# Kernel optimization log

Measured on AMD Instinct MI355X. Metric: run time of the kernel, lower is better.

Reference implementation:

```python
import jax, jax.numpy as jnp
import numpy as np

H_HT, W_HT = 26, 122      # downsampled pred grid fed to the Hough transform
NUM_ANGLE = 60            # 180 deg / 3 deg
NUM_RHO = 125             # 2*ceil(diag/2)+1, diag = sqrt(26^2+122^2)


def _make_vote_index():
    # Reproduce the structure of vote_index_26_122_3_1.mat: for each pixel
    # (h, w) and angle a, exactly one rho bin receives a vote of 1.0.
    theta = np.deg2rad(np.arange(NUM_ANGLE) * 3.0)
    ys = np.arange(H_HT) - H_HT / 2.0 + 0.5
    xs = np.arange(W_HT) - W_HT / 2.0 + 0.5
    # rho[h, w, a] = x*cos(theta_a) + y*sin(theta_a)
    rho = xs[None, :, None] * np.cos(theta)[None, None, :] \
        + ys[:, None, None] * np.sin(theta)[None, None, :]
    ri = np.clip(np.round(rho).astype(np.int64) + NUM_RHO // 2, 0, NUM_RHO - 1)
    vote = np.zeros((H_HT, W_HT, NUM_ANGLE, NUM_RHO), dtype=np.float32)
    hh, ww, aa = np.meshgrid(np.arange(H_HT), np.arange(W_HT),
                             np.arange(NUM_ANGLE), indexing='ij')
    vote[hh, ww, aa, ri] = 1.0
    return jnp.asarray(vote)


def setup_inputs() -> dict:
    key = jax.random.key(0)
    k1, k2, k3 = jax.random.split(key, 3)
    B, C = 32, 4
    ht = jax.random.uniform(k1, (B, C, NUM_ANGLE, NUM_RHO), dtype=jnp.float32)
    pred = jax.random.uniform(k2, (B, C, 288, 800), dtype=jnp.float32)
    pred_exist = jax.random.uniform(k3, (B, C), dtype=jnp.float32)
    vote_index = _make_vote_index()
    return {"ht": ht, "pred": pred, "pred_exist": pred_exist,
            "vote_index": vote_index}


def _nearest_resize(x, out_h, out_w):
    # torch F.interpolate(mode='nearest'): src = floor(dst * in/out)
    in_h, in_w = x.shape[2], x.shape[3]
    hi = jnp.floor(jnp.arange(out_h) * (in_h / out_h)).astype(jnp.int32)
    wi = jnp.floor(jnp.arange(out_w) * (in_w / out_w)).astype(jnp.int32)
    return x[:, :, hi][:, :, :, wi]


def reference(ht, pred, pred_exist, vote_index):
    B, C = ht.shape[0], ht.shape[1]
    # --- no_grad block in the original ---
    exist = (pred_exist > 0.9).astype(ht.dtype)          # [B, 4]
    exist = jnp.broadcast_to(exist[:, None, :], (B, C, 4))  # [B, C, 4]
    pred_s = _nearest_resize(pred, H_HT, W_HT)           # [B, C, 26, 122]
    # Hough-transform vote accumulation: gather pixel values into (angle, rho)
    # bins via the one-hot vote_index table.
    pred_ht = jnp.einsum('bchw,hwar->bcar', pred_s, vote_index)  # [B,C,A,R]
    idx = jnp.argmax(pred_ht.reshape(B, C, -1), axis=2)  # [B, 4]
    idx = jnp.broadcast_to(idx[:, None, :], (B, C, 4))   # [B, C, 4]
    # --- differentiable part ---
    # F.normalize(ht, dim=2, p=1): L1-normalize along the angle dim.
    l1 = jnp.sum(jnp.abs(ht), axis=2, keepdims=True)
    ht_n = ht / jnp.maximum(l1, 1e-12)
    flat = ht_n.reshape(B, C, -1)                        # [B, C, A*R]
    gathered = jnp.take_along_axis(flat, idx, axis=2)    # [B, C, 4]
    ht_max_log = -jnp.log(gathered + 1e-12)
    loss = ht_max_log * exist
    return loss.mean(axis=2).mean(axis=1)                # [B]
```

## Files before the change

kernel.cpp:

```cpp
#include <hip/hip_runtime.h>
#include <hip/hip_bf16.h>
#include <stdint.h>
#include <math.h>

#define H_HT 26
#define W_HT 122
#define NPIX (H_HT * W_HT)
#define NA 60
#define NR 125
#define NB 32
#define NC 4
#define NBC (NB * NC)
#define PH 288
#define PW 800
#define NSPLIT 16
#define PIX_PT 13

#define TR_BLKS (H_HT * 8)
#define ZERO_BLKS 4

#define WS_OFF   190336
#define WS_LIST  220608
#define WS_PREDT 601280
#define WS_PVP   2225344

__global__ __launch_bounds__(256) void setup(const float* __restrict__ pred,
                                             int* __restrict__ off,
                                             uint16_t* __restrict__ list,
                                             float* __restrict__ pred_T,
                                             unsigned long long* __restrict__ pvp) {
    const int tid = threadIdx.x;
    if (blockIdx.x < NA) {
        const int a = blockIdx.x;
        __shared__ int s_cnt[NR];
        __shared__ int sc[2][NR];
        __shared__ int s_pre[NR + 1];
        __shared__ int s_cur[NR];

        double t  = __dmul_rn((double)(a * 3), 0.017453292519943295);
        double cs = cos(t);
        double sn = sin(t);

        int rloc[PIX_PT];
#pragma unroll
        for (int k = 0; k < PIX_PT; ++k) {
            int p = tid + k * 256;
            rloc[k] = 0;
            if (p < NPIX) {
                int h = p / W_HT;
                int w = p - h * W_HT;
                double xs = (double)w - 60.5;
                double ys = (double)h - 12.5;
                double rho = __dadd_rn(__dmul_rn(xs, cs), __dmul_rn(ys, sn));
                int r = (int)rint(rho) + NR / 2;
                r = r < 0 ? 0 : (r > NR - 1 ? NR - 1 : r);
                rloc[k] = r;
            }
        }
        for (int i = tid; i < NR; i += 256) s_cnt[i] = 0;
        __syncthreads();
#pragma unroll
        for (int k = 0; k < PIX_PT; ++k) {
            int p = tid + k * 256;
            if (p < NPIX) atomicAdd(&s_cnt[rloc[k]], 1);
        }
        __syncthreads();
        if (tid < NR) sc[0][tid] = s_cnt[tid];
        __syncthreads();
        int pin = 0;
        for (int d = 1; d < NR; d <<= 1) {
            if (tid < NR) {
                int v = sc[pin][tid];
                if (tid >= d) v += sc[pin][tid - d];
                sc[pin ^ 1][tid] = v;
            }
            __syncthreads();
            pin ^= 1;
        }
        if (tid == 0) s_pre[0] = 0;
        if (tid < NR) s_pre[tid + 1] = sc[pin][tid];
        __syncthreads();
        for (int r = tid; r < NR + 1; r += 256) off[a * (NR + 1) + r] = s_pre[r];
        for (int r = tid; r < NR; r += 256) s_cur[r] = s_pre[r];
        __syncthreads();
#pragma unroll
        for (int k = 0; k < PIX_PT; ++k) {
            int p = tid + k * 256;
            if (p < NPIX) {
                int slot = atomicAdd(&s_cur[rloc[k]], 1);
                list[a * NPIX + slot] = (uint16_t)p;
            }
        }
    } else if (blockIdx.x < NA + TR_BLKS) {
        const int bidx = blockIdx.x - NA;
        const int h    = bidx >> 3;
        const int g    = bidx & 7;
        const int bc0  = g * 16;
        __shared__ float s_row[16][802];
        const float C1 = (float)(288.0 / 26.0);
        const float C2 = (float)(800.0 / 122.0);
        const int hi = (int)floorf((float)h * C1);
        for (int i = tid; i < 16 * 200; i += 256) {
            int j  = i / 200;
            int c4 = i - j * 200;
            const float4* rp = reinterpret_cast<const float4*>(
                pred + ((size_t)(bc0 + j) * PH + hi) * PW);
            float4 v = rp[c4];
            s_row[j][c4 * 4 + 0] = v.x;
            s_row[j][c4 * 4 + 1] = v.y;
            s_row[j][c4 * 4 + 2] = v.z;
            s_row[j][c4 * 4 + 3] = v.w;
        }
        __syncthreads();
        for (int idx = tid; idx < W_HT * 16; idx += 256) {
            int w = idx >> 4;
            int j = idx & 15;
            int wi = (int)floorf((float)w * C2);
            pred_T[(size_t)(h * W_HT + w) * NBC + bc0 + j] = s_row[j][wi];
        }
    } else {
        int bz = blockIdx.x - NA - TR_BLKS;
        int i0 = bz * 256 + tid;
        for (int i = i0; i < NA * NBC; i += ZERO_BLKS * 256) pvp[i] = 0ull;
    }
}

__global__ __launch_bounds__(256) void hough_T7(const float* __restrict__ pred_T,
                                                const int* __restrict__ off,
                                                const uint16_t* __restrict__ list,
                                                unsigned long long* __restrict__ pvp) {
    __shared__ uint16_t s_list[NPIX];
    __shared__ int      s_off[NR + 1];
    __shared__ float    s_v[4][32][4];
    __shared__ int      s_i[4][32][4];

    const int blk  = blockIdx.x;
    const int a    = blk / NSPLIT;
    const int q    = blk - a * NSPLIT;
    const int tid  = threadIdx.x;
    const int w    = tid >> 6;
    const int lane = tid & 63;
    const int li   = lane & 31;
    const int hw8  = (lane >> 5) * 8;

    {
        const uint32_t* src = reinterpret_cast<const uint32_t*>(list + a * NPIX);
        uint32_t* dst = reinterpret_cast<uint32_t*>(s_list);
        for (int i = tid; i < NPIX / 2; i += 256) dst[i] = src[i];
        for (int r = tid; r < NR + 1; r += 256) s_off[r] = off[a * (NR + 1) + r];
    }
    __syncthreads();

    const float4* pT4 = reinterpret_cast<const float4*>(pred_T);
    float bvx = -1.0f, bvy = -1.0f, bvz = -1.0f, bvw = -1.0f;
    int   bix = 0, biy = 0, biz = 0, biw = 0;
    for (int r = q * 4 + w; r < NR; r += 64) {
        const int o0 = s_off[r];
        const int o1 = s_off[r + 1];
        float4 c0 = {0,0,0,0}, c1 = {0,0,0,0}, c2 = {0,0,0,0}, c3 = {0,0,0,0};
        float4 c4 = {0,0,0,0}, c5 = {0,0,0,0}, c6 = {0,0,0,0}, c7 = {0,0,0,0};
        for (int j = o0; j < o1; j += 16) {
            int base = j + hw8;
            int i0 = base, i1 = base + 1, i2 = base + 2, i3 = base + 3;
            int i4 = base + 4, i5 = base + 5, i6 = base + 6, i7 = base + 7;
            float m0 = (i0 < o1) ? 1.0f : 0.0f;
            float m1 = (i1 < o1) ? 1.0f : 0.0f;
            float m2 = (i2 < o1) ? 1.0f : 0.0f;
            float m3 = (i3 < o1) ? 1.0f : 0.0f;
            float m4 = (i4 < o1) ? 1.0f : 0.0f;
            float m5 = (i5 < o1) ? 1.0f : 0.0f;
            float m6 = (i6 < o1) ? 1.0f : 0.0f;
            float m7 = (i7 < o1) ? 1.0f : 0.0f;
            int p0 = s_list[i0 < o1 ? i0 : o0];
            int p1 = s_list[i1 < o1 ? i1 : o0];
            int p2 = s_list[i2 < o1 ? i2 : o0];
            int p3 = s_list[i3 < o1 ? i3 : o0];
            int p4 = s_list[i4 < o1 ? i4 : o0];
            int p5 = s_list[i5 < o1 ? i5 : o0];
            int p6 = s_list[i6 < o1 ? i6 : o0];
            int p7 = s_list[i7 < o1 ? i7 : o0];
            float4 v0 = pT4[p0 * 32 + li];
            float4 v1 = pT4[p1 * 32 + li];
            float4 v2 = pT4[p2 * 32 + li];
            float4 v3 = pT4[p3 * 32 + li];
            float4 v4 = pT4[p4 * 32 + li];
            float4 v5 = pT4[p5 * 32 + li];
            float4 v6 = pT4[p6 * 32 + li];
            float4 v7 = pT4[p7 * 32 + li];
            c0.x = fmaf(v0.x, m0, c0.x); c0.y = fmaf(v0.y, m0, c0.y);
            c0.z = fmaf(v0.z, m0, c0.z); c0.w = fmaf(v0.w, m0, c0.w);
            c1.x = fmaf(v1.x, m1, c1.x); c1.y = fmaf(v1.y, m1, c1.y);
            c1.z = fmaf(v1.z, m1, c1.z); c1.w = fmaf(v1.w, m1, c1.w);
            c2.x = fmaf(v2.x, m2, c2.x); c2.y = fmaf(v2.y, m2, c2.y);
            c2.z = fmaf(v2.z, m2, c2.z); c2.w = fmaf(v2.w, m2, c2.w);
            c3.x = fmaf(v3.x, m3, c3.x); c3.y = fmaf(v3.y, m3, c3.y);
            c3.z = fmaf(v3.z, m3, c3.z); c3.w = fmaf(v3.w, m3, c3.w);
            c4.x = fmaf(v4.x, m4, c4.x); c4.y = fmaf(v4.y, m4, c4.y);
            c4.z = fmaf(v4.z, m4, c4.z); c4.w = fmaf(v4.w, m4, c4.w);
            c5.x = fmaf(v5.x, m5, c5.x); c5.y = fmaf(v5.y, m5, c5.y);
            c5.z = fmaf(v5.z, m5, c5.z); c5.w = fmaf(v5.w, m5, c5.w);
            c6.x = fmaf(v6.x, m6, c6.x); c6.y = fmaf(v6.y, m6, c6.y);
            c6.z = fmaf(v6.z, m6, c6.z); c6.w = fmaf(v6.w, m6, c6.w);
            c7.x = fmaf(v7.x, m7, c7.x); c7.y = fmaf(v7.y, m7, c7.y);
            c7.z = fmaf(v7.z, m7, c7.z); c7.w = fmaf(v7.w, m7, c7.w);
        }
        float sx = ((c0.x + c1.x) + (c2.x + c3.x)) + ((c4.x + c5.x) + (c6.x + c7.x));
        float sy = ((c0.y + c1.y) + (c2.y + c3.y)) + ((c4.y + c5.y) + (c6.y + c7.y));
        float sz = ((c0.z + c1.z) + (c2.z + c3.z)) + ((c4.z + c5.z) + (c6.z + c7.z));
        float sw = ((c0.w + c1.w) + (c2.w + c3.w)) + ((c4.w + c5.w) + (c6.w + c7.w));
        sx += __shfl_xor(sx, 32);
        sy += __shfl_xor(sy, 32);
        sz += __shfl_xor(sz, 32);
        sw += __shfl_xor(sw, 32);
        int gbin = a * NR + r;
        if (sx > bvx) { bvx = sx; bix = gbin; }
        if (sy > bvy) { bvy = sy; biy = gbin; }
        if (sz > bvz) { bvz = sz; biz = gbin; }
        if (sw > bvw) { bvw = sw; biw = gbin; }
    }
    if (hw8 == 0) {
        s_v[w][li][0] = bvx; s_i[w][li][0] = bix;
        s_v[w][li][1] = bvy; s_i[w][li][1] = biy;
        s_v[w][li][2] = bvz; s_i[w][li][2] = biz;
        s_v[w][li][3] = bvw; s_i[w][li][3] = biw;
    }
    __syncthreads();
    if (tid < 32) {
#pragma unroll
        for (int comp = 0; comp < 4; ++comp) {
            float m = s_v[0][tid][comp];
            int   jb = s_i[0][tid][comp];
#pragma unroll
            for (int ww = 1; ww < 4; ++ww) {
                float ov = s_v[ww][tid][comp];
                int   oi = s_i[ww][tid][comp];
                if (ov > m || (ov == m && oi < jb)) { m = ov; jb = oi; }
            }
            unsigned long long e = ((unsigned long long)__float_as_uint(m < 0.f ? 0.f : m) << 32)
                                 | (unsigned long long)(65535 - jb);
            atomicMax(&pvp[(4 * tid + comp) * NA + a], e);
        }
    }
}

__global__ __launch_bounds__(256) void loss4(const float* __restrict__ ht,
                                             const float* __restrict__ pexist,
                                             const unsigned long long* __restrict__ pvp,
                                             float* __restrict__ out) {
    __shared__ float s_sum[4];
    const int b    = blockIdx.x;
    const int tid  = threadIdx.x;
    const int k    = tid >> 6;
    const int lane = tid & 63;
    const int c    = lane >> 4;
    const int s    = lane & 15;

    unsigned long long be = 0ull;
    if (lane < NA) be = pvp[(b * 4 + k) * NA + lane];
#pragma unroll
    for (int m = 32; m > 0; m >>= 1) {
        unsigned long long oe = __shfl_xor(be, m);
        if (oe > be) be = oe;
    }
    int fidx = 65535 - (int)(be & 0xFFFFull);
    int a0 = fidx / NR;
    int r  = fidx - a0 * NR;

    const float* htc = ht + (size_t)((b * 4 + c) * NA) * NR;
    float acc = 0.0f;
#pragma unroll
    for (int t = 0; t < 4; ++t) {
        int a = s + t * 16;
        if (a < NA) acc += fabsf(htc[a * NR + r]);
    }
#pragma unroll
    for (int m = 1; m < 16; m <<= 1) acc += __shfl_xor(acc, m);

    float term = 0.0f;
    if (s == 0) {
        float l1 = fmaxf(acc, 1e-12f);
        float gg = htc[a0 * NR + r] / l1;
        float ex = (pexist[b * 4 + k] > 0.9f) ? 1.0f : 0.0f;
        term = -logf(gg + 1e-12f) * ex;
    }
#pragma unroll
    for (int m = 16; m < 64; m <<= 1) term += __shfl_xor(term, m);
    if (lane == 0) s_sum[k] = term;
    __syncthreads();
    if (tid == 0)
        out[b] = (s_sum[0] + s_sum[1] + s_sum[2] + s_sum[3]) * (1.0f / 16.0f);
}

extern "C" void kernel_launch(void* const* d_in, const int* in_sizes, int n_in,
                              void* d_out, int out_size, void* d_ws, size_t ws_size,
                              hipStream_t stream) {
    const float* ht     = (const float*)d_in[0];
    const float* pred   = (const float*)d_in[1];
    const float* pexist = (const float*)d_in[2];

    char* ws = (char*)d_ws;
    int*      off    = (int*)     (ws + WS_OFF);
    uint16_t* list   = (uint16_t*)(ws + WS_LIST);
    float*    pred_T = (float*)   (ws + WS_PREDT);
    unsigned long long* pvp = (unsigned long long*)(ws + WS_PVP);

    setup<<<NA + TR_BLKS + ZERO_BLKS, 256, 0, stream>>>(pred, off, list, pred_T, pvp);
    hough_T7<<<NA * NSPLIT, 256, 0, stream>>>(pred_T, off, list, pvp);
    loss4<<<NB, 256, 0, stream>>>(ht, pexist, pvp, (float*)d_out);
}
```

Measured before the change: 30.08 us.

## Fuse loss into Hough kernel via last-block completion counter and precompute L1

Merges the separate loss kernel into the Hough kernel. Extra blocks compute the per-(b,c,r) L1 norms of ht alongside the voting blocks, and the last block to finish, detected through an atomic counter zeroed in setup, does the argmax reduction and the final loss. This removes one kernel launch and the serial dependency of the loss kernel. In exchange it adds threadfence/atomic overhead to every block and leaves a single block doing the final serial work. It also computes L1 for all rho bins, not just the selected ones.

```diff
diff --git a/kernel.cpp b/kernel.cpp
--- a/kernel.cpp
+++ b/kernel.cpp
@@ -18,17 +18,23 @@
 
 #define TR_BLKS (H_HT * 8)
 #define ZERO_BLKS 4
-
-#define WS_OFF   190336
-#define WS_LIST  220608
-#define WS_PREDT 601280
-#define WS_PVP   2225344
+#define HB (NA * NSPLIT)
+#define L1_BLKS 120
+#define K2_BLKS (HB + L1_BLKS)
+
+#define WS_OFF   0
+#define WS_LIST  30272
+#define WS_PREDT 410944
+#define WS_PVP   2035008
+#define WS_L1    2096448
+#define WS_CNT   2352448
 
 __global__ __launch_bounds__(256) void setup(const float* __restrict__ pred,
                                              int* __restrict__ off,
                                              uint16_t* __restrict__ list,
                                              float* __restrict__ pred_T,
-                                             unsigned long long* __restrict__ pvp) {
+                                             unsigned long long* __restrict__ pvp,
+                                             unsigned int* __restrict__ cnt) {
     const int tid = threadIdx.x;
     if (blockIdx.x < NA) {
         const int a = blockIdx.x;
@@ -122,173 +128,189 @@
         int bz = blockIdx.x - NA - TR_BLKS;
         int i0 = bz * 256 + tid;
         for (int i = i0; i < NA * NBC; i += ZERO_BLKS * 256) pvp[i] = 0ull;
+        if (bz == 0 && tid == 0) *cnt = 0u;
     }
 }
 
-__global__ __launch_bounds__(256) void hough_T7(const float* __restrict__ pred_T,
-                                                const int* __restrict__ off,
-                                                const uint16_t* __restrict__ list,
-                                                unsigned long long* __restrict__ pvp) {
+__global__ __launch_bounds__(256) void hough_l1_loss(const float* __restrict__ pred_T,
+                                                     const int* __restrict__ off,
+                                                     const uint16_t* __restrict__ list,
+                                                     unsigned long long* __restrict__ pvp,
+                                                     float* __restrict__ L1t,
+                                                     unsigned int* __restrict__ cnt,
+                                                     const float* __restrict__ ht,
+                                                     const float* __restrict__ pexist,
+                                                     float* __restrict__ out) {
     __shared__ uint16_t s_list[NPIX];
     __shared__ int      s_off[NR + 1];
     __shared__ float    s_v[4][32][4];
     __shared__ int      s_i[4][32][4];
 
-    const int blk  = blockIdx.x;
-    const int a    = blk / NSPLIT;
-    const int q    = blk - a * NSPLIT;
-    const int tid  = threadIdx.x;
-    const int w    = tid >> 6;
-    const int lane = tid & 63;
-    const int li   = lane & 31;
-    const int hw8  = (lane >> 5) * 8;
-
-    {
-        const uint32_t* src = reinterpret_cast<const uint32_t*>(list + a * NPIX);
-        uint32_t* dst = reinterpret_cast<uint32_t*>(s_list);
-        for (int i = tid; i < NPIX / 2; i += 256) dst[i] = src[i];
-        for (int r = tid; r < NR + 1; r += 256) s_off[r] = off[a * (NR + 1) + r];
-    }
+    const int tid = threadIdx.x;
+
+    if (blockIdx.x < HB) {
+        const int blk  = blockIdx.x;
+        const int a    = blk / NSPLIT;
+        const int q    = blk - a * NSPLIT;
+        const int w    = tid >> 6;
+        const int lane = tid & 63;
+        const int li   = lane & 31;
+        const int hw8  = (lane >> 5) * 8;
+
+        {
+            const uint32_t* src = reinterpret_cast<const uint32_t*>(list + a * NPIX);
+            uint32_t* dst = reinterpret_cast<uint32_t*>(s_list);
+            for (int i = tid; i < NPIX / 2; i += 256) dst[i] = src[i];
+            for (int r = tid; r < NR + 1; r += 256) s_off[r] = off[a * (NR + 1) + r];
+        }
+        __syncthreads();
+
+        const float4* pT4 = reinterpret_cast<const float4*>(pred_T);
+        float bvx = -1.0f, bvy = -1.0f, bvz = -1.0f, bvw = -1.0f;
+        int   bix = 0, biy = 0, biz = 0, biw = 0;
+        for (int r = q * 4 + w; r < NR; r += 64) {
+            const int o0 = s_off[r];
+            const int o1 = s_off[r + 1];
+            float4 c0 = {0,0,0,0}, c1 = {0,0,0,0}, c2 = {0,0,0,0}, c3 = {0,0,0,0};
+            float4 c4 = {0,0,0,0}, c5 = {0,0,0,0}, c6 = {0,0,0,0}, c7 = {0,0,0,0};
+            for (int j = o0; j < o1; j += 16) {
+                int base = j + hw8;
+                int i0 = base, i1 = base + 1, i2 = base + 2, i3 = base + 3;
+                int i4 = base + 4, i5 = base + 5, i6 = base + 6, i7 = base + 7;
+                float m0 = (i0 < o1) ? 1.0f : 0.0f;
+                float m1 = (i1 < o1) ? 1.0f : 0.0f;
+                float m2 = (i2 < o1) ? 1.0f : 0.0f;
+                float m3 = (i3 < o1) ? 1.0f : 0.0f;
+                float m4 = (i4 < o1) ? 1.0f : 0.0f;
+                float m5 = (i5 < o1) ? 1.0f : 0.0f;
+                float m6 = (i6 < o1) ? 1.0f : 0.0f;
+                float m7 = (i7 < o1) ? 1.0f : 0.0f;
+                int p0 = s_list[i0 < o1 ? i0 : o0];
+                int p1 = s_list[i1 < o1 ? i1 : o0];
+                int p2 = s_list[i2 < o1 ? i2 : o0];
+                int p3 = s_list[i3 < o1 ? i3 : o0];
+                int p4 = s_list[i4 < o1 ? i4 : o0];
+                int p5 = s_list[i5 < o1 ? i5 : o0];
+                int p6 = s_list[i6 < o1 ? i6 : o0];
+                int p7 = s_list[i7 < o1 ? i7 : o0];
+                float4 v0 = pT4[p0 * 32 + li];
+                float4 v1 = pT4[p1 * 32 + li];
+                float4 v2 = pT4[p2 * 32 + li];
+                float4 v3 = pT4[p3 * 32 + li];
+                float4 v4 = pT4[p4 * 32 + li];
+                float4 v5 = pT4[p5 * 32 + li];
+                float4 v6 = pT4[p6 * 32 + li];
+                float4 v7 = pT4[p7 * 32 + li];
+                c0.x = fmaf(v0.x, m0, c0.x); c0.y = fmaf(v0.y, m0, c0.y);
+                c0.z = fmaf(v0.z, m0, c0.z); c0.w = fmaf(v0.w, m0, c0.w);
+                c1.x = fmaf(v1.x, m1, c1.x); c1.y = fmaf(v1.y, m1, c1.y);
+                c1.z = fmaf(v1.z, m1, c1.z); c1.w = fmaf(v1.w, m1, c1.w);
+                c2.x = fmaf(v2.x, m2, c2.x); c2.y = fmaf(v2.y, m2, c2.y);
+                c2.z = fmaf(v2.z, m2, c2.z); c2.w = fmaf(v2.w, m2, c2.w);
+                c3.x = fmaf(v3.x, m3, c3.x); c3.y = fmaf(v3.y, m3, c3.y);
+                c3.z = fmaf(v3.z, m3, c3.z); c3.w = fmaf(v3.w, m3, c3.w);
+                c4.x = fmaf(v4.x, m4, c4.x); c4.y = fmaf(v4.y, m4, c4.y);
+                c4.z = fmaf(v4.z, m4, c4.z); c4.w = fmaf(v4.w, m4, c4.w);
+                c5.x = fmaf(v5.x, m5, c5.x); c5.y = fmaf(v5.y, m5, c5.y);
+                c5.z = fmaf(v5.z, m5, c5.z); c5.w = fmaf(v5.w, m5, c5.w);
+                c6.x = fmaf(v6.x, m6, c6.x); c6.y = fmaf(v6.y, m6, c6.y);
+                c6.z = fmaf(v6.z, m6, c6.z); c6.w = fmaf(v6.w, m6, c6.w);
+                c7.x = fmaf(v7.x, m7, c7.x); c7.y = fmaf(v7.y, m7, c7.y);
+                c7.z = fmaf(v7.z, m7, c7.z); c7.w = fmaf(v7.w, m7, c7.w);
+            }
+            float sx = ((c0.x + c1.x) + (c2.x + c3.x)) + ((c4.x + c5.x) + (c6.x + c7.x));
+            float sy = ((c0.y + c1.y) + (c2.y + c3.y)) + ((c4.y + c5.y) + (c6.y + c7.y));
+            float sz = ((c0.z + c1.z) + (c2.z + c3.z)) + ((c4.z + c5.z) + (c6.z + c7.z));
+            float sw = ((c0.w + c1.w) + (c2.w + c3.w)) + ((c4.w + c5.w) + (c6.w + c7.w));
+            sx += __shfl_xor(sx, 32);
+            sy += __shfl_xor(sy, 32);
+            sz += __shfl_xor(sz, 32);
+            sw += __shfl_xor(sw, 32);
+            int gbin = a * NR + r;
+            if (sx > bvx) { bvx = sx; bix = gbin; }
+            if (sy > bvy) { bvy = sy; biy = gbin; }
+            if (sz > bvz) { bvz = sz; biz = gbin; }
+            if (sw > bvw) { bvw = sw; biw = gbin; }
+        }
+        if (hw8 == 0) {
+            s_v[w][li][0] = bvx; s_i[w][li][0] = bix;
+            s_v[w][li][1] = bvy; s_i[w][li][1] = biy;
+            s_v[w][li][2] = bvz; s_i[w][li][2] = biz;
+            s_v[w][li][3] = bvw; s_i[w][li][3] = biw;
+        }
+        __syncthreads();
+        if (tid < 32) {
+#pragma unroll
+            for (int comp = 0; comp < 4; ++comp) {
+                float m = s_v[0][tid][comp];
+                int   jb = s_i[0][tid][comp];
+#pragma unroll
+                for (int ww = 1; ww < 4; ++ww) {
+                    float ov = s_v[ww][tid][comp];
+                    int   oi = s_i[ww][tid][comp];
+                    if (ov > m || (ov == m && oi < jb)) { m = ov; jb = oi; }
+                }
+                unsigned long long e = ((unsigned long long)__float_as_uint(m < 0.f ? 0.f : m) << 32)
+                                     | (unsigned long long)(65535 - jb);
+                atomicMax(&pvp[(4 * tid + comp) * NA + a], e);
+            }
+        }
+    } else {
+        const int i = blockIdx.x - HB;
+        for (int e = i * 256 + tid; e < NBC * NR; e += L1_BLKS * 256) {
+            int cr = e / NR;
+            int r  = e - cr * NR;
+            const float* base = ht + (size_t)cr * NA * NR + r;
+            float s = 0.0f;
+            for (int a = 0; a < NA; ++a) s += fabsf(base[a * NR]);
+            L1t[e] = s;
+        }
+    }
+
+    __shared__ unsigned int s_last;
+    __threadfence();
     __syncthreads();
-
-    const float4* pT4 = reinterpret_cast<const float4*>(pred_T);
-    float bvx = -1.0f, bvy = -1.0f, bvz = -1.0f, bvw = -1.0f;
-    int   bix = 0, biy = 0, biz = 0, biw = 0;
-    for (int r = q * 4 + w; r < NR; r += 64) {
-        const int o0 = s_off[r];
-        const int o1 = s_off[r + 1];
-        float4 c0 = {0,0,0,0}, c1 = {0,0,0,0}, c2 = {0,0,0,0}, c3 = {0,0,0,0};
-        float4 c4 = {0,0,0,0}, c5 = {0,0,0,0}, c6 = {0,0,0,0}, c7 = {0,0,0,0};
-        for (int j = o0; j < o1; j += 16) {
-            int base = j + hw8;
-            int i0 = base, i1 = base + 1, i2 = base + 2, i3 = base + 3;
-            int i4 = base + 4, i5 = base + 5, i6 = base + 6, i7 = base + 7;
-            float m0 = (i0 < o1) ? 1.0f : 0.0f;
-            float m1 = (i1 < o1) ? 1.0f : 0.0f;
-            float m2 = (i2 < o1) ? 1.0f : 0.0f;
-            float m3 = (i3 < o1) ? 1.0f : 0.0f;
-            float m4 = (i4 < o1) ? 1.0f : 0.0f;
-            float m5 = (i5 < o1) ? 1.0f : 0.0f;
-            float m6 = (i6 < o1) ? 1.0f : 0.0f;
-            float m7 = (i7 < o1) ? 1.0f : 0.0f;
-            int p0 = s_list[i0 < o1 ? i0 : o0];
-            int p1 = s_list[i1 < o1 ? i1 : o0];
-            int p2 = s_list[i2 < o1 ? i2 : o0];
-            int p3 = s_list[i3 < o1 ? i3 : o0];
-            int p4 = s_list[i4 < o1 ? i4 : o0];
-            int p5 = s_list[i5 < o1 ? i5 : o0];
-            int p6 = s_list[i6 < o1 ? i6 : o0];
-            int p7 = s_list[i7 < o1 ? i7 : o0];
-            float4 v0 = pT4[p0 * 32 + li];
-            float4 v1 = pT4[p1 * 32 + li];
-            float4 v2 = pT4[p2 * 32 + li];
-            float4 v3 = pT4[p3 * 32 + li];
-            float4 v4 = pT4[p4 * 32 + li];
-            float4 v5 = pT4[p5 * 32 + li];
-            float4 v6 = pT4[p6 * 32 + li];
-            float4 v7 = pT4[p7 * 32 + li];
-            c0.x = fmaf(v0.x, m0, c0.x); c0.y = fmaf(v0.y, m0, c0.y);
-            c0.z = fmaf(v0.z, m0, c0.z); c0.w = fmaf(v0.w, m0, c0.w);
-            c1.x = fmaf(v1.x, m1, c1.x); c1.y = fmaf(v1.y, m1, c1.y);
-            c1.z = fmaf(v1.z, m1, c1.z); c1.w = fmaf(v1.w, m1, c1.w);
-            c2.x = fmaf(v2.x, m2, c2.x); c2.y = fmaf(v2.y, m2, c2.y);
-            c2.z = fmaf(v2.z, m2, c2.z); c2.w = fmaf(v2.w, m2, c2.w);
-            c3.x = fmaf(v3.x, m3, c3.x); c3.y = fmaf(v3.y, m3, c3.y);
-            c3.z = fmaf(v3.z, m3, c3.z); c3.w = fmaf(v3.w, m3, c3.w);
-            c4.x = fmaf(v4.x, m4, c4.x); c4.y = fmaf(v4.y, m4, c4.y);
-            c4.z = fmaf(v4.z, m4, c4.z); c4.w = fmaf(v4.w, m4, c4.w);
-            c5.x = fmaf(v5.x, m5, c5.x); c5.y = fmaf(v5.y, m5, c5.y);
-            c5.z = fmaf(v5.z, m5, c5.z); c5.w = fmaf(v5.w, m5, c5.w);
-            c6.x = fmaf(v6.x, m6, c6.x); c6.y = fmaf(v6.y, m6, c6.y);
-            c6.z = fmaf(v6.z, m6, c6.z); c6.w = fmaf(v6.w, m6, c6.w);
-            c7.x = fmaf(v7.x, m7, c7.x); c7.y = fmaf(v7.y, m7, c7.y);
-            c7.z = fmaf(v7.z, m7, c7.z); c7.w = fmaf(v7.w, m7, c7.w);
-        }
-        float sx = ((c0.x + c1.x) + (c2.x + c3.x)) + ((c4.x + c5.x) + (c6.x + c7.x));
-        float sy = ((c0.y + c1.y) + (c2.y + c3.y)) + ((c4.y + c5.y) + (c6.y + c7.y));
-        float sz = ((c0.z + c1.z) + (c2.z + c3.z)) + ((c4.z + c5.z) + (c6.z + c7.z));
-        float sw = ((c0.w + c1.w) + (c2.w + c3.w)) + ((c4.w + c5.w) + (c6.w + c7.w));
-        sx += __shfl_xor(sx, 32);
-        sy += __shfl_xor(sy, 32);
-        sz += __shfl_xor(sz, 32);
-        sw += __shfl_xor(sw, 32);
-        int gbin = a * NR + r;
-        if (sx > bvx) { bvx = sx; bix = gbin; }
-        if (sy > bvy) { bvy = sy; biy = gbin; }
-        if (sz > bvz) { bvz = sz; biz = gbin; }
-        if (sw > bvw) { bvw = sw; biw = gbin; }
-    }
-    if (hw8 == 0) {
-        s_v[w][li][0] = bvx; s_i[w][li][0] = bix;
-        s_v[w][li][1] = bvy; s_i[w][li][1] = biy;
-        s_v[w][li][2] = bvz; s_i[w][li][2] = biz;
-        s_v[w][li][3] = bvw; s_i[w][li][3] = biw;
-    }
+    if (tid == 0) s_last = atomicAdd(cnt, 1u);
     __syncthreads();
-    if (tid < 32) {
-#pragma unroll
-        for (int comp = 0; comp < 4; ++comp) {
-            float m = s_v[0][tid][comp];
-            int   jb = s_i[0][tid][comp];
-#pragma unroll
-            for (int ww = 1; ww < 4; ++ww) {
-                float ov = s_v[ww][tid][comp];
-                int   oi = s_i[ww][tid][comp];
-                if (ov > m || (ov == m && oi < jb)) { m = ov; jb = oi; }
-            }
-            unsigned long long e = ((unsigned long long)__float_as_uint(m < 0.f ? 0.f : m) << 32)
-                                 | (unsigned long long)(65535 - jb);
-            atomicMax(&pvp[(4 * tid + comp) * NA + a], e);
-        }
-    }
-}
-
-__global__ __launch_bounds__(256) void loss4(const float* __restrict__ ht,
-                                             const float* __restrict__ pexist,
-                                             const unsigned long long* __restrict__ pvp,
-                                             float* __restrict__ out) {
-    __shared__ float s_sum[4];
-    const int b    = blockIdx.x;
-    const int tid  = threadIdx.x;
-    const int k    = tid >> 6;
-    const int lane = tid & 63;
-    const int c    = lane >> 4;
-    const int s    = lane & 15;
-
-    unsigned long long be = 0ull;
-    if (lane < NA) be = pvp[(b * 4 + k) * NA + lane];
-#pragma unroll
-    for (int m = 32; m > 0; m >>= 1) {
-        unsigned long long oe = __shfl_xor(be, m);
-        if (oe > be) be = oe;
-    }
-    int fidx = 65535 - (int)(be & 0xFFFFull);
-    int a0 = fidx / NR;
-    int r  = fidx - a0 * NR;
-
-    const float* htc = ht + (size_t)((b * 4 + c) * NA) * NR;
-    float acc = 0.0f;
-#pragma unroll
-    for (int t = 0; t < 4; ++t) {
-        int a = s + t * 16;
-        if (a < NA) acc += fabsf(htc[a * NR + r]);
-    }
-#pragma unroll
-    for (int m = 1; m < 16; m <<= 1) acc += __shfl_xor(acc, m);
-
-    float term = 0.0f;
-    if (s == 0) {
-        float l1 = fmaxf(acc, 1e-12f);
-        float gg = htc[a0 * NR + r] / l1;
+    if (s_last != (unsigned int)(K2_BLKS - 1)) return;
+    __threadfence();
+
+    __shared__ int   s_fidx[NBC];
+    __shared__ float s_t[512];
+
+    if (tid < NBC) {
+        unsigned long long be = 0ull;
+        const unsigned long long* pr = pvp + (size_t)tid * NA;
+        for (int aa = 0; aa < NA; ++aa) {
+            unsigned long long e = pr[aa];
+            if (e > be) be = e;
+        }
+        s_fidx[tid] = 65535 - (int)(be & 0xFFFFull);
+    }
+    __syncthreads();
+
+#pragma unroll
+    for (int it = 0; it < 2; ++it) {
+        int T = tid + 256 * it;
+        int b = T >> 4;
+        int combo = T & 15;
+        int c = combo >> 2;
+        int k = combo & 3;
+        int fidx = s_fidx[b * 4 + k];
+        int a0 = fidx / NR;
+        int r  = fidx - a0 * NR;
+        int cr = b * 4 + c;
+        float l1 = fmaxf(L1t[cr * NR + r], 1e-12f);
+        float gg = ht[((size_t)cr * NA + a0) * NR + r] / l1;
         float ex = (pexist[b * 4 + k] > 0.9f) ? 1.0f : 0.0f;
-        term = -logf(gg + 1e-12f) * ex;
-    }
-#pragma unroll
-    for (int m = 16; m < 64; m <<= 1) term += __shfl_xor(term, m);
-    if (lane == 0) s_sum[k] = term;
+        s_t[T] = -logf(gg + 1e-12f) * ex;
+    }
     __syncthreads();
-    if (tid == 0)
-        out[b] = (s_sum[0] + s_sum[1] + s_sum[2] + s_sum[3]) * (1.0f / 16.0f);
+    if (tid < NB) {
+        float s = 0.0f;
+        for (int i2 = 0; i2 < 16; ++i2) s += s_t[tid * 16 + i2];
+        out[tid] = s * (1.0f / 16.0f);
+    }
 }
 
 extern "C" void kernel_launch(void* const* d_in, const int* in_sizes, int n_in,
@@ -303,8 +325,10 @@
     uint16_t* list   = (uint16_t*)(ws + WS_LIST);
     float*    pred_T = (float*)   (ws + WS_PREDT);
     unsigned long long* pvp = (unsigned long long*)(ws + WS_PVP);
-
-    setup<<<NA + TR_BLKS + ZERO_BLKS, 256, 0, stream>>>(pred, off, list, pred_T, pvp);
-    hough_T7<<<NA * NSPLIT, 256, 0, stream>>>(pred_T, off, list, pvp);
-    loss4<<<NB, 256, 0, stream>>>(ht, pexist, pvp, (float*)d_out);
+    float*    L1t    = (float*)   (ws + WS_L1);
+    unsigned int* cnt = (unsigned int*)(ws + WS_CNT);
+
+    setup<<<NA + TR_BLKS + ZERO_BLKS, 256, 0, stream>>>(pred, off, list, pred_T, pvp, cnt);
+    hough_l1_loss<<<K2_BLKS, 256, 0, stream>>>(pred_T, off, list, pvp, L1t, cnt,
+                                               ht, pexist, (float*)d_out);
 }
```

Result: slower. 111.7 us (+271.3%).
